# Performance work log

Measured on AMD Instinct MI355X. Metric: run time of the kernel, lower is better.

Reference implementation:

```python
import jax, jax.numpy as jnp
import numpy as np

B, S, D_DEC, D_ENC, F, U = 64, 8192, 128, 128, 16, 128
CLIP_C = 10.0
BIG_NUMBER = 1e9


def setup_inputs() -> dict:
    key = jax.random.key(0)
    ks = jax.random.split(key, 10)
    scale = 1.0 / np.sqrt(U)
    return {
        "dec_output": jax.random.normal(ks[0], (B, 1, D_DEC), dtype=jnp.float32),
        "enc_input": jax.random.normal(ks[1], (B, S, F), dtype=jnp.float32),
        "enc_outputs": jax.random.normal(ks[2], (B, S, D_ENC), dtype=jnp.float32),
        "mask": jax.random.bernoulli(ks[3], 0.3, (B, S)).astype(jnp.float32),
        "W1_w": jax.random.uniform(ks[4], (D_DEC, U), jnp.float32, -scale, scale),
        "W1_b": jnp.zeros((U,), jnp.float32),
        "W2_w": jax.random.uniform(ks[5], (D_ENC, U), jnp.float32, -scale, scale),
        "W2_b": jnp.zeros((U,), jnp.float32),
        "V_w": jax.random.uniform(ks[6], (U, 1), jnp.float32, -scale, scale),
        "V_b": jnp.zeros((1,), jnp.float32),
    }


def reference(dec_output, enc_input, enc_outputs, mask, W1_w, W1_b, W2_w, W2_b, V_w, V_b):
    # dec_output: [B,1,Ddec] (already has time dim; add_time_dim=False)
    q = dec_output @ W1_w + W1_b                  # [B,1,U]
    k = enc_outputs @ W2_w + W2_b                 # [B,S,U]
    score = jnp.tanh(q + k) @ V_w + V_b           # [B,S,1]
    pointer_logits = jnp.squeeze(score, axis=2)   # [B,S]
    pointer_logits = CLIP_C * jnp.tanh(pointer_logits)
    pointer_logits = pointer_logits - mask * BIG_NUMBER
    pointer_probs = jax.nn.softmax(pointer_logits, axis=-1)
    pointer_index = jnp.argmax(pointer_probs, axis=-1).astype(jnp.int32)  # [B]
    gathered = enc_input[jnp.arange(enc_input.shape[0]), pointer_index]   # [B,F]
    return (pointer_logits, pointer_probs, pointer_index, gathered)
```

## Files before the change

### kernel.cpp

```cpp
#include <hip/hip_runtime.h>
#include <cmath>

constexpr int Bn   = 64;
constexpr int Sn   = 8192;
constexpr int DDEC = 128;
constexpr int DENC = 128;
constexpr int Fn   = 16;
constexpr int Un   = 128;

using bf16x8 = __attribute__((ext_vector_type(8))) short;
using f32x4  = __attribute__((ext_vector_type(4))) float;

__device__ __forceinline__ float fast_tanh(float x) {
    float ax = fabsf(x);
    float e  = __expf(2.0f * ax);
    float t  = 1.0f - 2.0f * __builtin_amdgcn_rcpf(e + 1.0f);
    return copysignf(t, x);
}

__device__ __forceinline__ unsigned int fkey(float f) {
    unsigned int u = __float_as_uint(f);
    return (u & 0x80000000u) ? ~u : (u | 0x80000000u);
}

__device__ __forceinline__ unsigned int bf16_rne(float f) {
    unsigned int u = __float_as_uint(f);
    return (u + 0x7FFFu + ((u >> 16) & 1u)) >> 16;
}

__global__ void setup_kernel(const float* __restrict__ dec,
                             const float* __restrict__ W1,
                             const float* __restrict__ W1b,
                             const float* __restrict__ W2,
                             const float* __restrict__ W2b,
                             float* __restrict__ qq,
                             uint4* __restrict__ wftab,
                             float* __restrict__ sums,
                             unsigned long long* __restrict__ amax) {
    int blk = blockIdx.x, tid = threadIdx.x;
    if (blk < Bn) {
        if (tid < Un) {
            int b = blk, u = tid;
            float acc = W1b[u] + W2b[u];
            #pragma unroll 8
            for (int d = 0; d < DDEC; ++d)
                acc = fmaf(dec[b * DDEC + d], W1[d * Un + u], acc);
            qq[b * Un + u] = acc;
        }
        if (tid == 0) { sums[blk] = 0.0f; amax[blk] = 0ull; }
    } else {
        int n = blk - Bn;
        int c = tid >> 6;
        int lane = tid & 63;
        int d0 = c * 32 + (lane >> 4) * 8;
        int u  = n * 16 + (lane & 15);
        unsigned int r[8];
        #pragma unroll
        for (int t = 0; t < 8; ++t)
            r[t] = bf16_rne(W2[(d0 + t) * Un + u]);
        uint4 out;
        out.x = r[0] | (r[1] << 16);
        out.y = r[2] | (r[3] << 16);
        out.z = r[4] | (r[5] << 16);
        out.w = r[6] | (r[7] << 16);
        wftab[(n * 4 + c) * 64 + lane] = out;
    }
}

__device__ __forceinline__ void cvt_hilo(float4 a, float4 b, uint4& hi, uint4& lo) {
    unsigned int ua[8] = { __float_as_uint(a.x), __float_as_uint(a.y),
                           __float_as_uint(a.z), __float_as_uint(a.w),
                           __float_as_uint(b.x), __float_as_uint(b.y),
                           __float_as_uint(b.z), __float_as_uint(b.w) };
    float fa[8] = { a.x, a.y, a.z, a.w, b.x, b.y, b.z, b.w };
    unsigned int vl[8];
    #pragma unroll
    for (int j = 0; j < 8; ++j) {
        float hf = __uint_as_float(ua[j] & 0xFFFF0000u);
        vl[j] = __float_as_uint(fa[j] - hf);
    }
    hi.x = (ua[1] & 0xFFFF0000u) | (ua[0] >> 16);
    hi.y = (ua[3] & 0xFFFF0000u) | (ua[2] >> 16);
    hi.z = (ua[5] & 0xFFFF0000u) | (ua[4] >> 16);
    hi.w = (ua[7] & 0xFFFF0000u) | (ua[6] >> 16);
    lo.x = (vl[1] & 0xFFFF0000u) | (vl[0] >> 16);
    lo.y = (vl[3] & 0xFFFF0000u) | (vl[2] >> 16);
    lo.z = (vl[5] & 0xFFFF0000u) | (vl[4] >> 16);
    lo.w = (vl[7] & 0xFFFF0000u) | (vl[6] >> 16);
}

__global__ __launch_bounds__(256, 2)
void score_kernel(const float* __restrict__ enc,
                  const float* __restrict__ mask,
                  const float* __restrict__ qq,
                  const uint4* __restrict__ wftab,
                  const float* __restrict__ V,
                  const float* __restrict__ Vb,
                  float* __restrict__ logits,
                  float* __restrict__ probs,
                  float* __restrict__ sums,
                  unsigned long long* __restrict__ amax) {
    const int tid  = threadIdx.x;
    const int lane = tid & 63;
    const int wv   = tid >> 6;
    const int wave_id = blockIdx.x * 4 + wv;
    const int base = wave_id * 256;
    const int b    = base >> 13;
    const int g    = lane >> 4;
    const int li   = lane & 15;

    uint4 wf[32];
    #pragma unroll
    for (int i = 0; i < 32; ++i) wf[i] = wftab[i * 64 + lane];

    float qv[8], Vl[8];
    #pragma unroll
    for (int n = 0; n < 8; ++n) {
        qv[n] = qq[b * Un + n * 16 + li];
        Vl[n] = V[n * 16 + li];
    }
    const float Vbias = Vb[0];
    const bool active = (li < 4);

    const float4* eptr = (const float4*)enc;
    float4 ebuf[8];
    {
        size_t i0 = (size_t)(base + li) * 32 + g * 2;
        #pragma unroll
        for (int c = 0; c < 4; ++c) {
            ebuf[2 * c]     = eptr[i0 + c * 8];
            ebuf[2 * c + 1] = eptr[i0 + c * 8 + 1];
        }
    }

    float psum = 0.0f;
    unsigned long long key = 0ull;

    #pragma unroll 1
    for (int st = 0; st < 16; ++st) {
        const int myrow = base + st * 16 + 4 * g + li;
        float mval = 0.0f;
        if (active) mval = mask[myrow];

        uint4 fh[4], fl[4];
        #pragma unroll
        for (int c = 0; c < 4; ++c)
            cvt_hilo(ebuf[2 * c], ebuf[2 * c + 1], fh[c], fl[c]);

        if (st < 15) {
            size_t i0 = (size_t)(base + (st + 1) * 16 + li) * 32 + g * 2;
            #pragma unroll
            for (int c = 0; c < 4; ++c) {
                ebuf[2 * c]     = eptr[i0 + c * 8];
                ebuf[2 * c + 1] = eptr[i0 + c * 8 + 1];
            }
        }

        f32x4 acc[8];
        #pragma unroll
        for (int n = 0; n < 8; ++n)
            acc[n] = f32x4{qv[n], qv[n], qv[n], qv[n]};
        #pragma unroll
        for (int c = 0; c < 4; ++c) {
            bf16x8 ah = __builtin_bit_cast(bf16x8, fh[c]);
            bf16x8 al = __builtin_bit_cast(bf16x8, fl[c]);
            #pragma unroll
            for (int n = 0; n < 8; ++n)
                acc[n] = __builtin_amdgcn_mfma_f32_16x16x32_bf16(
                    ah, __builtin_bit_cast(bf16x8, wf[n * 4 + c]), acc[n], 0, 0, 0);
            #pragma unroll
            for (int n = 0; n < 8; ++n)
                acc[n] = __builtin_amdgcn_mfma_f32_16x16x32_bf16(
                    al, __builtin_bit_cast(bf16x8, wf[n * 4 + c]), acc[n], 0, 0, 0);
        }

        float pr0 = 0.0f, pr1 = 0.0f, pr2 = 0.0f, pr3 = 0.0f;
        #pragma unroll
        for (int n = 0; n < 8; ++n) {
            pr0 = fmaf(fast_tanh(acc[n][0]), Vl[n], pr0);
            pr1 = fmaf(fast_tanh(acc[n][1]), Vl[n], pr1);
            pr2 = fmaf(fast_tanh(acc[n][2]), Vl[n], pr2);
            pr3 = fmaf(fast_tanh(acc[n][3]), Vl[n], pr3);
        }
        #pragma unroll
        for (int off = 1; off < 16; off <<= 1) {
            pr0 += __shfl_xor(pr0, off);
            pr1 += __shfl_xor(pr1, off);
            pr2 += __shfl_xor(pr2, off);
            pr3 += __shfl_xor(pr3, off);
        }
        if (active) {
            float sc = (li == 0) ? pr0 : (li == 1) ? pr1 : (li == 2) ? pr2 : pr3;
            sc += Vbias;
            float l = 10.0f * fast_tanh(sc) - mval * 1e9f;
            logits[myrow] = l;
            float p = __expf(l - 10.0f);
            probs[myrow] = p;
            psum += p;
            unsigned long long k =
                ((unsigned long long)fkey(l) << 32) |
                (unsigned int)(Sn - 1 - (myrow & (Sn - 1)));
            if (k > key) key = k;
        }
    }

    #pragma unroll
    for (int off = 1; off < 64; off <<= 1) {
        psum += __shfl_xor(psum, off);
        unsigned long long ok = __shfl_xor(key, off);
        if (ok > key) key = ok;
    }
    if (lane == 0) {
        atomicAdd(&sums[b], psum);
        atomicMax(&amax[b], key);
    }
}

__global__ __launch_bounds__(256)
void finalize_kernel(const float* __restrict__ logits,
                     const float* __restrict__ enc,
                     const float* __restrict__ qq,
                     const float* __restrict__ W2,
                     const float* __restrict__ V,
                     const float* __restrict__ Vb,
                     const float* __restrict__ enc_in,
                     const float* __restrict__ sums,
                     const unsigned long long* __restrict__ amax,
                     float* __restrict__ probs,
                     float* __restrict__ out_idx,
                     float* __restrict__ out_gath) {
    int blk = blockIdx.x;
    int tid = threadIdx.x;
    if (blk < (Bn * Sn) / (256 * 4)) {
        int i4 = blk * 256 + tid;
        int b = i4 >> 11;
        float inv = 1.0f / sums[b];
        float4* p4 = (float4*)probs;
        float4 v = p4[i4];
        v.x *= inv; v.y *= inv; v.z *= inv; v.w *= inv;
        p4[i4] = v;
        return;
    }
    int b = blk - (Bn * Sn) / (256 * 4);

    __shared__ int cnt;
    __shared__ int cand[64];
    __shared__ float red[256];
    __shared__ float bestL;
    __shared__ int bestI;
    if (tid == 0) { cnt = 0; bestL = -INFINITY; bestI = 0x7fffffff; }
    __syncthreads();

    unsigned int hk = (unsigned int)(amax[b] >> 32);
    float M = (hk & 0x80000000u) ? __uint_as_float(hk & 0x7FFFFFFFu)
                                 : __uint_as_float(~hk);
    const float* lrow = logits + (size_t)b * Sn;
    for (int s = tid; s < Sn; s += 256) {
        if (lrow[s] >= M - 0.125f) {
            int i = atomicAdd(&cnt, 1);
            if (i < 64) cand[i] = s;
        }
    }
    __syncthreads();
    int n = min(cnt, 64);
    int u = tid & 127, h = tid >> 7;

    for (int c = 0; c < n; ++c) {
        int row_s = cand[c];
        const float* erow = enc + ((size_t)b * Sn + row_s) * DENC;
        float kp = 0.0f;
        #pragma unroll 8
        for (int dd = 0; dd < 64; ++dd) {
            int d = h * 64 + dd;
            kp = fmaf(erow[d], W2[d * Un + u], kp);
        }
        red[tid] = kp;
        __syncthreads();
        if (tid < 128) {
            float kk = red[tid] + red[tid + 128] + qq[b * Un + tid];
            red[tid] = fast_tanh(kk) * V[tid];
        }
        __syncthreads();
        for (int off = 64; off > 0; off >>= 1) {
            if (tid < off) red[tid] += red[tid + off];
            __syncthreads();
        }
        if (tid == 0) {
            float sc = red[0] + Vb[0];
            float l = 10.0f * fast_tanh(sc);
            if (l > bestL || (l == bestL && row_s < bestI)) { bestL = l; bestI = row_s; }
        }
        __syncthreads();
    }

    if (tid == 0) out_idx[b] = (float)bestI;
    __syncthreads();
    if (tid < Fn) out_gath[b * Fn + tid] = enc_in[((size_t)b * Sn + bestI) * Fn + tid];
}

extern "C" void kernel_launch(void* const* d_in, const int* in_sizes, int n_in,
                              void* d_out, int out_size, void* d_ws, size_t ws_size,
                              hipStream_t stream) {
    const float* dec    = (const float*)d_in[0];
    const float* enc_in = (const float*)d_in[1];
    const float* enc    = (const float*)d_in[2];
    const float* mask   = (const float*)d_in[3];
    const float* W1     = (const float*)d_in[4];
    const float* W1b    = (const float*)d_in[5];
    const float* W2     = (const float*)d_in[6];
    const float* W2b    = (const float*)d_in[7];
    const float* V      = (const float*)d_in[8];
    const float* Vb     = (const float*)d_in[9];

    float* qq   = (float*)d_ws;
    float* sums = qq + Bn * Un;
    unsigned long long* amax =
        (unsigned long long*)(sums + Bn);
    uint4* wftab = (uint4*)(amax + Bn);

    float* logits = (float*)d_out;
    float* probs  = logits + (size_t)Bn * Sn;
    float* oidx   = probs + (size_t)Bn * Sn;
    float* ogath  = oidx + Bn;

    setup_kernel<<<Bn + 8, 256, 0, stream>>>(dec, W1, W1b, W2, W2b, qq, wftab, sums, amax);
    score_kernel<<<(Bn * Sn) / (256 * 4), 256, 0, stream>>>(
        enc, mask, qq, wftab, V, Vb, logits, probs, sums, amax);
    finalize_kernel<<<(Bn * Sn) / (256 * 4) + Bn, 256, 0, stream>>>(
        logits, enc, qq, W2, V, Vb, enc_in, sums, amax, probs, oidx, ogath);
}
```

Before: 439.3 us.

## Stage W2 fragments in LDS and halve rows per wave for occupancy

Moves the 32 per-lane weight fragments from registers into shared memory, loaded once per block, and reads them inside the MFMA loop. This frees about 128 VGPRs so launch bounds can target 3 blocks per SIMD. Rows per wave drop from 256 to 128 and the grid doubles. The hi/lo conversion is fused into the MFMA loop, and the next-tile prefetch now comes after the MFMAs. The trade is extra LDS reads per MFMA, more per-block setup, and a possibly weaker load/compute overlap.

```diff
diff --git a/kernel.cpp b/kernel.cpp
--- a/kernel.cpp
+++ b/kernel.cpp
@@ -7,6 +7,10 @@
 constexpr int DENC = 128;
 constexpr int Fn   = 16;
 constexpr int Un   = 128;
+
+constexpr int ROWS_PER_WAVE  = 128;
+constexpr int ROWS_PER_BLOCK = 512;
+constexpr int NSUB = ROWS_PER_WAVE / 16;
 
 using bf16x8 = __attribute__((ext_vector_type(8))) short;
 using f32x4  = __attribute__((ext_vector_type(4))) float;
@@ -89,7 +93,7 @@
     lo.w = (vl[7] & 0xFFFF0000u) | (vl[6] >> 16);
 }
 
-__global__ __launch_bounds__(256, 2)
+__global__ __launch_bounds__(256, 3)
 void score_kernel(const float* __restrict__ enc,
                   const float* __restrict__ mask,
                   const float* __restrict__ qq,
@@ -100,18 +104,18 @@
                   float* __restrict__ probs,
                   float* __restrict__ sums,
                   unsigned long long* __restrict__ amax) {
+    __shared__ uint4 wlds[32 * 64];
     const int tid  = threadIdx.x;
     const int lane = tid & 63;
     const int wv   = tid >> 6;
-    const int wave_id = blockIdx.x * 4 + wv;
-    const int base = wave_id * 256;
-    const int b    = base >> 13;
+    const int base = blockIdx.x * ROWS_PER_BLOCK + wv * ROWS_PER_WAVE;
+    const int b    = blockIdx.x >> 4;
     const int g    = lane >> 4;
     const int li   = lane & 15;
 
-    uint4 wf[32];
     #pragma unroll
-    for (int i = 0; i < 32; ++i) wf[i] = wftab[i * 64 + lane];
+    for (int it = 0; it < 8; ++it)
+        wlds[tid + it * 256] = wftab[tid + it * 256];
 
     float qv[8], Vl[8];
     #pragma unroll
@@ -122,6 +126,8 @@
     const float Vbias = Vb[0];
     const bool active = (li < 4);
 
+    __syncthreads();
+
     const float4* eptr = (const float4*)enc;
     float4 ebuf[8];
     {
@@ -137,41 +143,37 @@
     unsigned long long key = 0ull;
 
     #pragma unroll 1
-    for (int st = 0; st < 16; ++st) {
+    for (int st = 0; st < NSUB; ++st) {
         const int myrow = base + st * 16 + 4 * g + li;
         float mval = 0.0f;
         if (active) mval = mask[myrow];
 
-        uint4 fh[4], fl[4];
-        #pragma unroll
-        for (int c = 0; c < 4; ++c)
-            cvt_hilo(ebuf[2 * c], ebuf[2 * c + 1], fh[c], fl[c]);
-
-        if (st < 15) {
+        f32x4 acc[8];
+        #pragma unroll
+        for (int n = 0; n < 8; ++n)
+            acc[n] = f32x4{qv[n], qv[n], qv[n], qv[n]};
+
+        #pragma unroll
+        for (int c = 0; c < 4; ++c) {
+            uint4 hi, lo;
+            cvt_hilo(ebuf[2 * c], ebuf[2 * c + 1], hi, lo);
+            bf16x8 ah = __builtin_bit_cast(bf16x8, hi);
+            bf16x8 al = __builtin_bit_cast(bf16x8, lo);
+            #pragma unroll
+            for (int n = 0; n < 8; ++n) {
+                bf16x8 bf = __builtin_bit_cast(bf16x8, wlds[(n * 4 + c) * 64 + lane]);
+                acc[n] = __builtin_amdgcn_mfma_f32_16x16x32_bf16(ah, bf, acc[n], 0, 0, 0);
+                acc[n] = __builtin_amdgcn_mfma_f32_16x16x32_bf16(al, bf, acc[n], 0, 0, 0);
+            }
+        }
+
+        if (st < NSUB - 1) {
             size_t i0 = (size_t)(base + (st + 1) * 16 + li) * 32 + g * 2;
             #pragma unroll
             for (int c = 0; c < 4; ++c) {
                 ebuf[2 * c]     = eptr[i0 + c * 8];
                 ebuf[2 * c + 1] = eptr[i0 + c * 8 + 1];
             }
-        }
-
-        f32x4 acc[8];
-        #pragma unroll
-        for (int n = 0; n < 8; ++n)
-            acc[n] = f32x4{qv[n], qv[n], qv[n], qv[n]};
-        #pragma unroll
-        for (int c = 0; c < 4; ++c) {
-            bf16x8 ah = __builtin_bit_cast(bf16x8, fh[c]);
-            bf16x8 al = __builtin_bit_cast(bf16x8, fl[c]);
-            #pragma unroll
-            for (int n = 0; n < 8; ++n)
-                acc[n] = __builtin_amdgcn_mfma_f32_16x16x32_bf16(
-                    ah, __builtin_bit_cast(bf16x8, wf[n * 4 + c]), acc[n], 0, 0, 0);
-            #pragma unroll
-            for (int n = 0; n < 8; ++n)
-                acc[n] = __builtin_amdgcn_mfma_f32_16x16x32_bf16(
-                    al, __builtin_bit_cast(bf16x8, wf[n * 4 + c]), acc[n], 0, 0, 0);
         }
 
         float pr0 = 0.0f, pr1 = 0.0f, pr2 = 0.0f, pr3 = 0.0f;
@@ -324,7 +326,7 @@
     float* ogath  = oidx + Bn;
 
     setup_kernel<<<Bn + 8, 256, 0, stream>>>(dec, W1, W1b, W2, W2b, qq, wftab, sums, amax);
-    score_kernel<<<(Bn * Sn) / (256 * 4), 256, 0, stream>>>(
+    score_kernel<<<(Bn * Sn) / ROWS_PER_BLOCK, 256, 0, stream>>>(
         enc, mask, qq, wftab, V, Vb, logits, probs, sums, amax);
     finalize_kernel<<<(Bn * Sn) / (256 * 4) + Bn, 256, 0, stream>>>(
         logits, enc, qq, W2, V, Vb, enc_in, sums, amax, probs, oidx, ogath);
```

Result: slower. 577.9 us (+31.6%).
